# Performance work log

Hardware: AMD Instinct MI355X
Metric: run time of the kernel (lower is better)

The kernel has to match this reference:

```python
import jax, jax.numpy as jnp
import numpy as np

DIM, HEADS, MLP_RATIO = 384, 6, 4.0
HEAD_DIM = DIM // HEADS
HID = int(DIM * MLP_RATIO)
EPS = 1e-5


def _layer_norm(x, g, b):
    m = jnp.mean(x, axis=-1, keepdims=True)
    v = jnp.mean(jnp.square(x - m), axis=-1, keepdims=True)
    return (x - m) * jax.lax.rsqrt(v + EPS) * g + b


def setup_inputs() -> dict:
    key = jax.random.key(0)
    ks = jax.random.split(key, 16)
    B, N, C = 4, 2048, DIM
    s = 0.02
    return {
        "x": jax.random.normal(ks[0], (B, N, C), dtype=jnp.float32),
        "ln1_g": jnp.ones((C,), jnp.float32),
        "ln1_b": jnp.zeros((C,), jnp.float32),
        "qkv_w": jax.random.normal(ks[1], (C, 3 * C), jnp.float32) * s,  # [in, out]
        "qkv_b": jnp.zeros((3 * C,), jnp.float32),
        "proj_w": jax.random.normal(ks[2], (C, C), jnp.float32) * s,
        "proj_b": jnp.zeros((C,), jnp.float32),
        "ln2_g": jnp.ones((C,), jnp.float32),
        "ln2_b": jnp.zeros((C,), jnp.float32),
        "fc1_w": jax.random.normal(ks[3], (C, HID), jnp.float32) * s,
        "fc1_b": jnp.zeros((HID,), jnp.float32),
        "fc2_w": jax.random.normal(ks[4], (HID, C), jnp.float32) * s,
        "fc2_b": jnp.zeros((C,), jnp.float32),
    }


def reference(x, ln1_g, ln1_b, qkv_w, qkv_b, proj_w, proj_b,
              ln2_g, ln2_b, fc1_w, fc1_b, fc2_w, fc2_b):
    B, N, C = x.shape
    scale = HEAD_DIM ** (-0.5)

    # --- attention branch (pre-norm) ---
    h = _layer_norm(x, ln1_g, ln1_b)
    qkv = (h @ qkv_w + qkv_b).reshape(B, N, 3, HEADS, HEAD_DIM)
    qkv = jnp.transpose(qkv, (2, 0, 3, 1, 4))  # [3, B, H, N, D]
    q, k, v = qkv[0], qkv[1], qkv[2]
    attn = jnp.einsum("bhnd,bhmd->bhnm", q, k) * scale
    attn = jax.nn.softmax(attn, axis=-1)
    out = jnp.einsum("bhnm,bhmd->bhnd", attn, v)
    out = jnp.transpose(out, (0, 2, 1, 3)).reshape(B, N, C)
    x = x + (out @ proj_w + proj_b)

    # --- MLP branch (pre-norm) ---
    h = _layer_norm(x, ln2_g, ln2_b)
    h = jax.nn.gelu(h @ fc1_w + fc1_b, approximate=False)
    x = x + (h @ fc2_w + fc2_b)
    return x
```

## Files before the change

### kernel.cpp

```cpp
#include <hip/hip_runtime.h>

typedef unsigned short u16;
typedef unsigned int u32;
typedef __bf16 bf16x8_t __attribute__((ext_vector_type(8)));
typedef float f32x4 __attribute__((ext_vector_type(4)));
typedef float f32x16 __attribute__((ext_vector_type(16)));

__device__ __forceinline__ u16 f2b(float f) {
  union { float f; u32 u; } v; v.f = f;
  u32 r = v.u + 0x7fffu + ((v.u >> 16) & 1u);
  return (u16)(r >> 16);
}

__device__ __forceinline__ u32 pkbf(float a, float b) {
  union { __bf16 h[2]; u32 u; } v;
  v.h[0] = (__bf16)a; v.h[1] = (__bf16)b;
  return v.u;
}

__device__ __forceinline__ size_t fmoff(int r, int c, int Kd) {
  return ((size_t)(r >> 4) * (Kd >> 3) + (c >> 3)) * 128 + (r & 15) * 8 + (c & 7);
}

__device__ __forceinline__ f32x4 mfma16(uint4 a, uint4 b, f32x4 c) {
  return __builtin_amdgcn_mfma_f32_16x16x32_bf16(
      __builtin_bit_cast(bf16x8_t, a), __builtin_bit_cast(bf16x8_t, b), c, 0, 0, 0);
}

__device__ __forceinline__ f32x16 mfma32(uint4 a, uint4 b, f32x16 c) {
  return __builtin_amdgcn_mfma_f32_32x32x16_bf16(
      __builtin_bit_cast(bf16x8_t, a), __builtin_bit_cast(bf16x8_t, b), c, 0, 0, 0);
}

__device__ __forceinline__ void plswap(u32& a, u32& b) {
  asm("v_permlane32_swap_b32 %0, %1" : "+v"(a), "+v"(b));
}

__device__ __forceinline__ void load_lds16(const void* g, void* l) {
  __builtin_amdgcn_global_load_lds(
      (const __attribute__((address_space(1))) unsigned int*)g,
      (__attribute__((address_space(3))) unsigned int*)l, 16, 0, 0);
}

template <int N>
__device__ __forceinline__ void waitvm() {
  if constexpr (N == 0) asm volatile("s_waitcnt vmcnt(0)" ::: "memory");
  else if constexpr (N == 4) asm volatile("s_waitcnt vmcnt(4)" ::: "memory");
  else if constexpr (N == 6) asm volatile("s_waitcnt vmcnt(6)" ::: "memory");
  else if constexpr (N == 8) asm volatile("s_waitcnt vmcnt(8)" ::: "memory");
  else asm volatile("s_waitcnt vmcnt(10)" ::: "memory");
}

__device__ __forceinline__ void ln_body(const float* __restrict__ x,
                                        const float* __restrict__ g,
                                        const float* __restrict__ bta,
                                        u16* __restrict__ out, int row,
                                        int lane) {
  const float* xr = x + (size_t)row * 384;
  float v[6];
  float s = 0.f;
#pragma unroll
  for (int i = 0; i < 6; i++) { v[i] = xr[i * 64 + lane]; s += v[i]; }
#pragma unroll
  for (int off = 32; off >= 1; off >>= 1) s += __shfl_xor(s, off);
  float mean = s * (1.0f / 384.0f);
  float vs = 0.f;
#pragma unroll
  for (int i = 0; i < 6; i++) { float d = v[i] - mean; vs += d * d; }
#pragma unroll
  for (int off = 32; off >= 1; off >>= 1) vs += __shfl_xor(vs, off);
  float rstd = rsqrtf(vs * (1.0f / 384.0f) + 1e-5f);
#pragma unroll
  for (int i = 0; i < 6; i++) {
    int c = i * 64 + lane;
    out[fmoff(row, c, 384)] = f2b((v[i] - mean) * rstd * g[c] + bta[c]);
  }
}

__global__ __launch_bounds__(256) void ln_k(const float* __restrict__ x,
                                            const float* __restrict__ g,
                                            const float* __restrict__ bta,
                                            u16* __restrict__ out) {
  ln_body(x, g, bta, out, blockIdx.x * 4 + (threadIdx.x >> 6),
          threadIdx.x & 63);
}

__global__ __launch_bounds__(256) void prep_k(
    const float* __restrict__ w0, u16* __restrict__ t0_,
    const float* __restrict__ w1, u16* __restrict__ t1_,
    const float* __restrict__ w2, u16* __restrict__ t2_,
    const float* __restrict__ w3, u16* __restrict__ t3_,
    const float* __restrict__ x, const float* __restrict__ g,
    const float* __restrict__ bta, u16* __restrict__ lnout) {
  __shared__ u16 L[64][68];
  int tile = blockIdx.x, tid = threadIdx.x;
  if (tile >= 432) {
    ln_body(x, g, bta, lnout, (tile - 432) * 4 + (tid >> 6), tid & 63);
    return;
  }
  const float* w; u16* wt; int K, N, rel; bool fm;
  if (tile < 108)      { w = w0; wt = t0_; K = 384;  N = 1152; rel = tile;       fm = false; }
  else if (tile < 144) { w = w1; wt = t1_; K = 384;  N = 384;  rel = tile - 108; fm = true; }
  else if (tile < 288) { w = w2; wt = t2_; K = 384;  N = 1536; rel = tile - 144; fm = false; }
  else                 { w = w3; wt = t3_; K = 1536; N = 384;  rel = tile - 288; fm = true; }
  int ntx = N >> 6;
  int tk = (rel / ntx) << 6, tn = (rel - (rel / ntx) * ntx) << 6;

  int r = tid >> 2, c0 = (tid & 3) << 4;
  const float* src = w + (size_t)(tk + r) * N + tn + c0;
#pragma unroll
  for (int j = 0; j < 16; j += 4) {
    float4 a = *(const float4*)(src + j);
    L[r][c0 + j + 0] = f2b(a.x);
    L[r][c0 + j + 1] = f2b(a.y);
    L[r][c0 + j + 2] = f2b(a.z);
    L[r][c0 + j + 3] = f2b(a.w);
  }
  __syncthreads();
  int n = tid >> 2, k0 = (tid & 3) << 4;
  u16 tmp[16];
#pragma unroll
  for (int j = 0; j < 16; j++) tmp[j] = L[k0 + j][n];
  if (fm) {
    u16* dst = wt + fmoff(tn + n, tk + k0, K);
    *(uint4*)dst = *(const uint4*)(tmp);
    *(uint4*)(dst + 128) = *(const uint4*)(tmp + 8);
  } else {
    u16* dst = wt + (size_t)(tn + n) * K + tk + k0;
    *(uint4*)dst = *(const uint4*)(tmp);
    *(uint4*)(dst + 8) = *(const uint4*)(tmp + 8);
  }
}

template <int EPI, int MR, int KD, int NX, int MINW>
__global__ __launch_bounds__(256, MINW) void gemm_k(
    const u16* __restrict__ A, const u16* __restrict__ Bt,
    const float* __restrict__ bias, const float* __restrict__ res,
    void* __restrict__ outp, int Nn,
    u16* __restrict__ qp, u16* __restrict__ kp, u16* __restrict__ vtp) {
  constexpr int NS = KD / 64;
  constexpr int KD8 = KD / 8;
  __shared__ __align__(16) u16 Bs[3][64 * 64];
  int tid = threadIdx.x;
  int lane = tid & 63, wid = tid >> 6;
  int li = lane & 15, lg = lane >> 4;
  int wr = wid >> 1, wc = wid & 1;

  int p = blockIdx.x;
  int idx = p >> 3;
  int cx = idx % NX;
  int row0 = ((p & 7) + ((idx / NX) << 3)) * (MR * 32);
  int col0 = cx * 64;

  int lr = lane >> 3;
  int sc8 = ((lane & 7) ^ lr) * 8;

  const u16* Ab = A + ((size_t)(row0 / 16 + wr * MR) * KD8 + lg) * 128 + li * 8;

  f32x4 z = {0.f, 0.f, 0.f, 0.f};
  f32x4 acc[MR][2];
#pragma unroll
  for (int m = 0; m < MR; m++)
#pragma unroll
    for (int n = 0; n < 2; n++) acc[m][n] = z;

  uint4 af0[MR][2], af1[MR][2];

  auto stageB = [&](int buf, int k0) {
#pragma unroll
    for (int j = 0; j < 2; j++) {
      int ib = wid * 2 + j;
      load_lds16(Bt + (size_t)(col0 + ib * 8 + lr) * KD + k0 + sc8,
                 (char*)Bs[buf] + ib * 1024);
    }
  };
  auto loadA = [&](uint4 (*dst)[2], int t) {
#pragma unroll
    for (int m = 0; m < MR; m++)
#pragma unroll
      for (int kk = 0; kk < 2; kk++)
        dst[m][kk] =
            *(const uint4*)(Ab + ((size_t)m * KD8 + t * 8 + kk * 4) * 128);
  };

  stageB(0, 0);
  stageB(1, 64);
  loadA(af0, 0);
  if (NS > 1) loadA(af1, 1);
  waitvm<2 * MR>();
  __builtin_amdgcn_s_barrier();
  asm volatile("" ::: "memory");

#pragma unroll
  for (int t = 0; t < NS; t++) {
    if (t + 2 < NS) stageB((t + 2) % 3, (t + 2) * 64);
    const char* Bsb = (const char*)Bs[t % 3];
#pragma unroll
    for (int kk = 0; kk < 2; kk++) {
      uint4 bf[2];
#pragma unroll
      for (int n = 0; n < 2; n++) {
        int c = wc * 32 + n * 16 + li;
        bf[n] = *(const uint4*)(Bsb + c * 128 +
                                ((kk * 64 + lg * 16) ^ ((c & 7) << 4)));
      }
#pragma unroll
      for (int m = 0; m < MR; m++)
#pragma unroll
        for (int n = 0; n < 2; n++)
          acc[m][n] = mfma16((t & 1) ? af1[m][kk] : af0[m][kk], bf[n],
                             acc[m][n]);
    }
    if (t + 2 < NS) {
      if (t & 1) loadA(af1, t + 2);
      else       loadA(af0, t + 2);
      waitvm<2 + 2 * MR>();
      __builtin_amdgcn_s_barrier();
      asm volatile("" ::: "memory");
    } else if (t + 1 < NS) {
      waitvm<0>();
      __builtin_amdgcn_s_barrier();
      asm volatile("" ::: "memory");
    }
  }

#pragma unroll
  for (int m = 0; m < MR; m++) {
#pragma unroll
    for (int n = 0; n < 2; n++) {
#pragma unroll
      for (int j = 0; j < 4; j++) {
        int r = row0 + wr * (MR * 16) + m * 16 + lg * 4 + j;
        int c = col0 + wc * 32 + n * 16 + li;
        float v = acc[m][n][j] + bias[c];
        if (EPI == 1) {
          float e = __expf(-1.5957691f * v * (1.f + 0.044715f * v * v));
          ((u16*)outp)[fmoff(r, c, Nn)] = f2b(v / (1.f + e));
        } else {
          int tt = c / 384;
          int c2 = c - tt * 384;
          int hh = c2 >> 6, d = c2 & 63;
          int bb = r >> 11, nn = r & 2047;
          size_t bh = (size_t)bb * 6 + hh;
          int tile = nn >> 5;
          if (tt == 2) {
            int kvl = nn & 31;
            int kvHalf = (kvl >> 4) & 1, h2 = (kvl >> 3) & 1, jj = kvl & 7;
            int dTile = d >> 5, l31 = d & 31;
            vtp[(((bh * 64 + tile) * 2 + dTile) * 2 + kvHalf) * 512 +
                (l31 + h2 * 32) * 8 + jj] = f2b(v);
          } else {
            int chunk = d >> 4, h2 = (d >> 3) & 1, e = d & 7;
            int l31 = nn & 31;
            size_t off = ((bh * 64 + tile) * 4 + chunk) * 512 +
                         (l31 + h2 * 32) * 8 + e;
            if (tt == 0) qp[off] = f2b(v * 0.18033688f);
            else         kp[off] = f2b(v);
          }
        }
      }
    }
  }
}

template <int KD, int NX, int MINW>
__global__ __launch_bounds__(256, MINW) void gemm_thin_k(
    const u16* __restrict__ A, const u16* __restrict__ Bt,
    const float* __restrict__ bias, const float* __restrict__ res,
    float* __restrict__ outp, int Nn) {
  constexpr int NS = KD / 64;
  constexpr int KD8 = KD / 8;
  int tid = threadIdx.x;
  int lane = tid & 63, wid = tid >> 6;
  int li = lane & 15, lg = lane >> 4;
  int wr = wid >> 1, wc = wid & 1;

  int p = blockIdx.x;
  int idx = p >> 3;
  int cx = idx % NX;
  int row0 = ((p & 7) + ((idx / NX) << 3)) * 64;
  int col0 = cx * 64;

  const u16* Ab = A + ((size_t)(row0 / 16 + wr * 2) * KD8 + lg) * 128 + li * 8;
  const u16* Bb = Bt + ((size_t)(col0 / 16 + wc * 2) * KD8 + lg) * 128 + li * 8;

  f32x4 z = {0.f, 0.f, 0.f, 0.f};
  f32x4 acc[2][2];
#pragma unroll
  for (int m = 0; m < 2; m++)
#pragma unroll
    for (int n = 0; n < 2; n++) acc[m][n] = z;

  uint4 af0[2][2], af1[2][2], bf0[2][2], bf1[2][2];

  auto loadA = [&](uint4 (*dst)[2], int t) {
#pragma unroll
    for (int m = 0; m < 2; m++)
#pragma unroll
      for (int kk = 0; kk < 2; kk++)
        dst[m][kk] =
            *(const uint4*)(Ab + ((size_t)m * KD8 + t * 8 + kk * 4) * 128);
  };
  auto loadB = [&](uint4 (*dst)[2], int t) {
#pragma unroll
    for (int n = 0; n < 2; n++)
#pragma unroll
      for (int kk = 0; kk < 2; kk++)
        dst[n][kk] =
            *(const uint4*)(Bb + ((size_t)n * KD8 + t * 8 + kk * 4) * 128);
  };

  loadA(af0, 0);
  loadB(bf0, 0);

#pragma unroll
  for (int t = 0; t < NS; t++) {
    if (t + 1 < NS) {
      if (t & 1) { loadA(af0, t + 1); loadB(bf0, t + 1); }
      else       { loadA(af1, t + 1); loadB(bf1, t + 1); }
    }
#pragma unroll
    for (int kk = 0; kk < 2; kk++)
#pragma unroll
      for (int m = 0; m < 2; m++)
#pragma unroll
        for (int n = 0; n < 2; n++)
          acc[m][n] = mfma16((t & 1) ? af1[m][kk] : af0[m][kk],
                             (t & 1) ? bf1[n][kk] : bf0[n][kk], acc[m][n]);
  }

#pragma unroll
  for (int m = 0; m < 2; m++)
#pragma unroll
    for (int n = 0; n < 2; n++)
#pragma unroll
      for (int j = 0; j < 4; j++) {
        int r = row0 + wr * 32 + m * 16 + lg * 4 + j;
        int c = col0 + wc * 32 + n * 16 + li;
        float v = acc[m][n][j] + bias[c];
        outp[(size_t)r * Nn + c] = v + res[(size_t)r * Nn + c];
      }
}

__global__ __launch_bounds__(256, 2) void attn_k(const u16* __restrict__ q,
                                                 const u16* __restrict__ k,
                                                 const u16* __restrict__ vt,
                                                 u16* __restrict__ out) {
  __shared__ __align__(16) float Ol[3][2][16][64];
  __shared__ float Ls[3][64];

  int tid = threadIdx.x;
  int lane = tid & 63, wid = tid >> 6;
  int l31 = lane & 31, hi = lane >> 5;
  int bid = blockIdx.x;
  int nid = (bid & 7) * 96 + (bid >> 3);
  int bh = nid >> 5, qT = nid & 31;
  int b = bh / 6, hh = bh - b * 6;
  int qb = qT * 64;

  const u16* qp_ = q + ((size_t)bh * 64 + qT * 2) * 2048 + lane * 8;
  const u16* kp_ = k + ((size_t)bh * 64 + wid * 16) * 2048 + lane * 8;
  const u16* vp_ = vt + ((size_t)bh * 64 + wid * 16) * 2048 + lane * 8;

  uint4 qf0[4], qf1[4], kf[4];
#pragma unroll
  for (int c = 0; c < 4; c++) qf0[c] = *(const uint4*)(qp_ + c * 512);
#pragma unroll
  for (int c = 0; c < 4; c++) qf1[c] = *(const uint4*)(qp_ + 2048 + c * 512);
#pragma unroll
  for (int c = 0; c < 4; c++) kf[c] = *(const uint4*)(kp_ + c * 512);
  kp_ += 2048;

  f32x16 o00, o01, o10, o11;
#pragma unroll
  for (int r = 0; r < 16; r++) {
    o00[r] = 0.f; o01[r] = 0.f; o10[r] = 0.f; o11[r] = 0.f;
  }
  float ls0 = 0.f, ls1 = 0.f;

#pragma unroll
  for (int t = 0; t < 16; t++) {
    uint4 vf0 = *(const uint4*)(vp_);
    uint4 vf1 = *(const uint4*)(vp_ + 512);
    uint4 vf2 = *(const uint4*)(vp_ + 1024);
    uint4 vf3 = *(const uint4*)(vp_ + 1536);
    uint4 kn[4];
    if (t < 15) {
#pragma unroll
      for (int c = 0; c < 4; c++) kn[c] = *(const uint4*)(kp_ + c * 512);
    }

    {
      f32x16 s;
#pragma unroll
      for (int r = 0; r < 16; r++) s[r] = 0.f;
#pragma unroll
      for (int c = 0; c < 4; c++) s = mfma32(kf[c], qf0[c], s);
      float p[16];
#pragma unroll
      for (int r = 0; r < 16; r++) p[r] = __builtin_amdgcn_exp2f(s[r]);
      ls0 += ((p[0] + p[1]) + (p[2] + p[3])) + ((p[4] + p[5]) + (p[6] + p[7])) +
             ((p[8] + p[9]) + (p[10] + p[11])) +
             ((p[12] + p[13]) + (p[14] + p[15]));
      u32 u[8];
#pragma unroll
      for (int i = 0; i < 8; i++) u[i] = pkbf(p[2 * i], p[2 * i + 1]);
      plswap(u[0], u[2]); plswap(u[1], u[3]);
      plswap(u[4], u[6]); plswap(u[5], u[7]);
      uint4 pa0 = {u[0], u[1], u[2], u[3]};
      uint4 pa1 = {u[4], u[5], u[6], u[7]};
      o00 = mfma32(pa0, vf0, o00);
      o00 = mfma32(pa1, vf1, o00);
      o01 = mfma32(pa0, vf2, o01);
      o01 = mfma32(pa1, vf3, o01);
    }
    {
      f32x16 s;
#pragma unroll
      for (int r = 0; r < 16; r++) s[r] = 0.f;
#pragma unroll
      for (int c = 0; c < 4; c++) s = mfma32(kf[c], qf1[c], s);
      float p[16];
#pragma unroll
      for (int r = 0; r < 16; r++) p[r] = __builtin_amdgcn_exp2f(s[r]);
      ls1 += ((p[0] + p[1]) + (p[2] + p[3])) + ((p[4] + p[5]) + (p[6] + p[7])) +
             ((p[8] + p[9]) + (p[10] + p[11])) +
             ((p[12] + p[13]) + (p[14] + p[15]));
      u32 u[8];
#pragma unroll
      for (int i = 0; i < 8; i++) u[i] = pkbf(p[2 * i], p[2 * i + 1]);
      plswap(u[0], u[2]); plswap(u[1], u[3]);
      plswap(u[4], u[6]); plswap(u[5], u[7]);
      uint4 pa0 = {u[0], u[1], u[2], u[3]};
      uint4 pa1 = {u[4], u[5], u[6], u[7]};
      o10 = mfma32(pa0, vf0, o10);
      o10 = mfma32(pa1, vf1, o10);
      o11 = mfma32(pa0, vf2, o11);
      o11 = mfma32(pa1, vf3, o11);
    }

    if (t < 15) {
#pragma unroll
      for (int c = 0; c < 4; c++) kf[c] = kn[c];
    }
    kp_ += 2048;
    vp_ += 2048;
  }

  ls0 += __shfl_xor(ls0, 32);
  ls1 += __shfl_xor(ls1, 32);

  if (wid) {
#pragma unroll
    for (int r = 0; r < 16; r++) {
      Ol[wid - 1][0][r][lane] = o00[r];
      Ol[wid - 1][1][r][lane] = o01[r];
    }
    Ls[wid - 1][lane] = ls0;
  }
  __syncthreads();
  if (wid == 0) {
#pragma unroll
    for (int w = 0; w < 3; w++) ls0 += Ls[w][lane];
#pragma unroll
    for (int r = 0; r < 16; r++)
#pragma unroll
      for (int w = 0; w < 3; w++) {
        o00[r] += Ol[w][0][r][lane];
        o01[r] += Ol[w][1][r][lane];
      }
    float rl = 1.0f / ls0;
#pragma unroll
    for (int r = 0; r < 16; r++) {
      int qo = (r & 3) + 8 * (r >> 2) + hi * 4;
      float rlq = __shfl(rl, qo, 64);
      int row = b * 2048 + qb + qo;
      out[fmoff(row, hh * 64 + l31, 384)] = f2b(o00[r] * rlq);
      out[fmoff(row, hh * 64 + 32 + l31, 384)] = f2b(o01[r] * rlq);
    }
  }
  __syncthreads();
  if (wid) {
#pragma unroll
    for (int r = 0; r < 16; r++) {
      Ol[wid - 1][0][r][lane] = o10[r];
      Ol[wid - 1][1][r][lane] = o11[r];
    }
    Ls[wid - 1][lane] = ls1;
  }
  __syncthreads();
  if (wid == 0) {
#pragma unroll
    for (int w = 0; w < 3; w++) ls1 += Ls[w][lane];
#pragma unroll
    for (int r = 0; r < 16; r++)
#pragma unroll
      for (int w = 0; w < 3; w++) {
        o10[r] += Ol[w][0][r][lane];
        o11[r] += Ol[w][1][r][lane];
      }
    float rl = 1.0f / ls1;
#pragma unroll
    for (int r = 0; r < 16; r++) {
      int qo = (r & 3) + 8 * (r >> 2) + hi * 4;
      float rlq = __shfl(rl, qo, 64);
      int row = b * 2048 + qb + 32 + qo;
      out[fmoff(row, hh * 64 + l31, 384)] = f2b(o10[r] * rlq);
      out[fmoff(row, hh * 64 + 32 + l31, 384)] = f2b(o11[r] * rlq);
    }
  }
}

extern "C" void kernel_launch(void* const* d_in, const int* in_sizes, int n_in,
                              void* d_out, int out_size, void* d_ws,
                              size_t ws_size, hipStream_t stream) {
  const float* x      = (const float*)d_in[0];
  const float* ln1_g  = (const float*)d_in[1];
  const float* ln1_b  = (const float*)d_in[2];
  const float* qkv_w  = (const float*)d_in[3];
  const float* qkv_b  = (const float*)d_in[4];
  const float* proj_w = (const float*)d_in[5];
  const float* proj_b = (const float*)d_in[6];
  const float* ln2_g  = (const float*)d_in[7];
  const float* ln2_b  = (const float*)d_in[8];
  const float* fc1_w  = (const float*)d_in[9];
  const float* fc1_b  = (const float*)d_in[10];
  const float* fc2_w  = (const float*)d_in[11];
  const float* fc2_b  = (const float*)d_in[12];
  float* out = (float*)d_out;

  char* p = (char*)d_ws;
  u16* qkvwt  = (u16*)p;  p += (size_t)1152 * 384 * 2;
  u16* projwt = (u16*)p;  p += (size_t)384 * 384 * 2;
  u16* fc1wt  = (u16*)p;  p += (size_t)1536 * 384 * 2;
  u16* fc2wt  = (u16*)p;  p += (size_t)384 * 1536 * 2;
  float* x1   = (float*)p; p += (size_t)8192 * 384 * 4;
  u16* reg1   = (u16*)p;  p += (size_t)8192 * 384 * 2;
  u16* reg2   = (u16*)p;  p += (size_t)8192 * 1536 * 2;
  u16* qd  = reg2;
  u16* kd  = reg2 + (size_t)24 * 2048 * 64;
  u16* vtd = kd + (size_t)24 * 2048 * 64;
  u16* h3  = reg2;

  prep_k<<<432 + 2048, 256, 0, stream>>>(qkv_w, qkvwt, proj_w, projwt,
                                         fc1_w, fc1wt, fc2_w, fc2wt,
                                         x, ln1_g, ln1_b, reg1);
  gemm_k<2, 4, 384, 18, 2><<<dim3(1152), 256, 0, stream>>>(
      reg1, qkvwt, qkv_b, nullptr, nullptr, 1152, qd, kd, vtd);
  attn_k<<<dim3(768), 256, 0, stream>>>(qd, kd, vtd, reg1);
  gemm_thin_k<384, 6, 4><<<dim3(768), 256, 0, stream>>>(
      reg1, projwt, proj_b, x, x1, 384);
  ln_k<<<2048, 256, 0, stream>>>(x1, ln2_g, ln2_b, reg1);
  gemm_k<1, 4, 384, 24, 2><<<dim3(1536), 256, 0, stream>>>(
      reg1, fc1wt, fc1_b, nullptr, h3, 1536, nullptr, nullptr, nullptr);
  gemm_thin_k<1536, 6, 4><<<dim3(768), 256, 0, stream>>>(
      h3, fc2wt, fc2_b, x1, out, 384);
}
```

Measured before the change: 124.6 us.

## Fuse projection GEMM, residual and LayerNorm2; route fc2 through generic gemm kernel

Replaces the thin projection GEMM and the separate LN2 kernel with one projln_k kernel. Each block computes 16 full 384-wide rows, adds bias and residual, writes x1, and computes the LayerNorm statistics through shuffles and shared memory before emitting the bf16 LN output. This removes one launch and the re-read of x1 from global memory. The fc2 GEMM now uses the general gemm_k template with a new fp32 residual epilogue, and the fc2 weight prep layout flag changes to match. The single-pass E[x^2]-mean^2 variance is less numerically robust, and the narrower row tiles cut weight reuse per block.

Measured after the change: 121.4 us. -2.6%, faster.

```diff
diff --git a/kernel.cpp b/kernel.cpp
--- a/kernel.cpp
+++ b/kernel.cpp
@@ -75,14 +75,6 @@
     int c = i * 64 + lane;
     out[fmoff(row, c, 384)] = f2b((v[i] - mean) * rstd * g[c] + bta[c]);
   }
-}
-
-__global__ __launch_bounds__(256) void ln_k(const float* __restrict__ x,
-                                            const float* __restrict__ g,
-                                            const float* __restrict__ bta,
-                                            u16* __restrict__ out) {
-  ln_body(x, g, bta, out, blockIdx.x * 4 + (threadIdx.x >> 6),
-          threadIdx.x & 63);
 }
 
 __global__ __launch_bounds__(256) void prep_k(
@@ -102,7 +94,7 @@
   if (tile < 108)      { w = w0; wt = t0_; K = 384;  N = 1152; rel = tile;       fm = false; }
   else if (tile < 144) { w = w1; wt = t1_; K = 384;  N = 384;  rel = tile - 108; fm = true; }
   else if (tile < 288) { w = w2; wt = t2_; K = 384;  N = 1536; rel = tile - 144; fm = false; }
-  else                 { w = w3; wt = t3_; K = 1536; N = 384;  rel = tile - 288; fm = true; }
+  else                 { w = w3; wt = t3_; K = 1536; N = 384;  rel = tile - 288; fm = false; }
   int ntx = N >> 6;
   int tk = (rel / ntx) << 6, tn = (rel - (rel / ntx) * ntx) << 6;
 
@@ -233,7 +225,9 @@
         int r = row0 + wr * (MR * 16) + m * 16 + lg * 4 + j;
         int c = col0 + wc * 32 + n * 16 + li;
         float v = acc[m][n][j] + bias[c];
-        if (EPI == 1) {
+        if (EPI == 0) {
+          ((float*)outp)[(size_t)r * Nn + c] = v + res[(size_t)r * Nn + c];
+        } else if (EPI == 1) {
           float e = __expf(-1.5957691f * v * (1.f + 0.044715f * v * v));
           ((u16*)outp)[fmoff(r, c, Nn)] = f2b(v / (1.f + e));
         } else {
@@ -263,83 +257,107 @@
   }
 }
 
-template <int KD, int NX, int MINW>
-__global__ __launch_bounds__(256, MINW) void gemm_thin_k(
+__global__ __launch_bounds__(256, 2) void projln_k(
     const u16* __restrict__ A, const u16* __restrict__ Bt,
-    const float* __restrict__ bias, const float* __restrict__ res,
-    float* __restrict__ outp, int Nn) {
-  constexpr int NS = KD / 64;
-  constexpr int KD8 = KD / 8;
+    const float* __restrict__ bias, const float* __restrict__ x,
+    const float* __restrict__ g2, const float* __restrict__ b2,
+    float* __restrict__ x1, u16* __restrict__ h2) {
+  __shared__ float Sm[4][16], Sv[4][16];
   int tid = threadIdx.x;
   int lane = tid & 63, wid = tid >> 6;
   int li = lane & 15, lg = lane >> 4;
-  int wr = wid >> 1, wc = wid & 1;
-
-  int p = blockIdx.x;
-  int idx = p >> 3;
-  int cx = idx % NX;
-  int row0 = ((p & 7) + ((idx / NX) << 3)) * 64;
-  int col0 = cx * 64;
-
-  const u16* Ab = A + ((size_t)(row0 / 16 + wr * 2) * KD8 + lg) * 128 + li * 8;
-  const u16* Bb = Bt + ((size_t)(col0 / 16 + wc * 2) * KD8 + lg) * 128 + li * 8;
+  int r0 = blockIdx.x * 16;
+
+  const u16* Ab = A + ((size_t)(r0 >> 4) * 48 + lg) * 128 + li * 8;
+  const u16* Bb = Bt + ((size_t)(wid * 6) * 48 + lg) * 128 + li * 8;
 
   f32x4 z = {0.f, 0.f, 0.f, 0.f};
-  f32x4 acc[2][2];
-#pragma unroll
-  for (int m = 0; m < 2; m++)
-#pragma unroll
-    for (int n = 0; n < 2; n++) acc[m][n] = z;
-
-  uint4 af0[2][2], af1[2][2], bf0[2][2], bf1[2][2];
-
-  auto loadA = [&](uint4 (*dst)[2], int t) {
-#pragma unroll
-    for (int m = 0; m < 2; m++)
-#pragma unroll
-      for (int kk = 0; kk < 2; kk++)
-        dst[m][kk] =
-            *(const uint4*)(Ab + ((size_t)m * KD8 + t * 8 + kk * 4) * 128);
+  f32x4 acc[6];
+#pragma unroll
+  for (int n = 0; n < 6; n++) acc[n] = z;
+
+  uint4 af0[2], af1[2], bf0[6][2], bf1[6][2];
+  auto loadA = [&](uint4* dst, int t) {
+#pragma unroll
+    for (int kk = 0; kk < 2; kk++)
+      dst[kk] = *(const uint4*)(Ab + ((size_t)t * 8 + kk * 4) * 128);
   };
   auto loadB = [&](uint4 (*dst)[2], int t) {
 #pragma unroll
-    for (int n = 0; n < 2; n++)
+    for (int n = 0; n < 6; n++)
 #pragma unroll
       for (int kk = 0; kk < 2; kk++)
         dst[n][kk] =
-            *(const uint4*)(Bb + ((size_t)n * KD8 + t * 8 + kk * 4) * 128);
+            *(const uint4*)(Bb + ((size_t)n * 48 + t * 8 + kk * 4) * 128);
   };
 
   loadA(af0, 0);
   loadB(bf0, 0);
-
-#pragma unroll
-  for (int t = 0; t < NS; t++) {
-    if (t + 1 < NS) {
+#pragma unroll
+  for (int t = 0; t < 6; t++) {
+    if (t + 1 < 6) {
       if (t & 1) { loadA(af0, t + 1); loadB(bf0, t + 1); }
       else       { loadA(af1, t + 1); loadB(bf1, t + 1); }
     }
 #pragma unroll
     for (int kk = 0; kk < 2; kk++)
 #pragma unroll
-      for (int m = 0; m < 2; m++)
-#pragma unroll
-        for (int n = 0; n < 2; n++)
-          acc[m][n] = mfma16((t & 1) ? af1[m][kk] : af0[m][kk],
-                             (t & 1) ? bf1[n][kk] : bf0[n][kk], acc[m][n]);
-  }
-
-#pragma unroll
-  for (int m = 0; m < 2; m++)
-#pragma unroll
-    for (int n = 0; n < 2; n++)
-#pragma unroll
-      for (int j = 0; j < 4; j++) {
-        int r = row0 + wr * 32 + m * 16 + lg * 4 + j;
-        int c = col0 + wc * 32 + n * 16 + li;
-        float v = acc[m][n][j] + bias[c];
-        outp[(size_t)r * Nn + c] = v + res[(size_t)r * Nn + c];
-      }
+      for (int n = 0; n < 6; n++)
+        acc[n] = mfma16((t & 1) ? af1[kk] : af0[kk],
+                        (t & 1) ? bf1[n][kk] : bf0[n][kk], acc[n]);
+  }
+
+  float vv[6][4];
+  float s1[4] = {0.f, 0.f, 0.f, 0.f}, s2[4] = {0.f, 0.f, 0.f, 0.f};
+#pragma unroll
+  for (int n = 0; n < 6; n++) {
+    int c = wid * 96 + n * 16 + li;
+    float bc = bias[c];
+#pragma unroll
+    for (int j = 0; j < 4; j++) {
+      int r = r0 + lg * 4 + j;
+      float v = acc[n][j] + bc + x[(size_t)r * 384 + c];
+      vv[n][j] = v;
+      x1[(size_t)r * 384 + c] = v;
+      s1[j] += v;
+      s2[j] += v * v;
+    }
+  }
+#pragma unroll
+  for (int off = 8; off >= 1; off >>= 1)
+#pragma unroll
+    for (int j = 0; j < 4; j++) {
+      s1[j] += __shfl_xor(s1[j], off);
+      s2[j] += __shfl_xor(s2[j], off);
+    }
+  if (li == 0) {
+#pragma unroll
+    for (int j = 0; j < 4; j++) {
+      Sm[wid][lg * 4 + j] = s1[j];
+      Sv[wid][lg * 4 + j] = s2[j];
+    }
+  }
+  __syncthreads();
+  float mean[4], rstd[4];
+#pragma unroll
+  for (int j = 0; j < 4; j++) {
+    int rr = lg * 4 + j;
+    float t1 = (Sm[0][rr] + Sm[1][rr]) + (Sm[2][rr] + Sm[3][rr]);
+    float t2 = (Sv[0][rr] + Sv[1][rr]) + (Sv[2][rr] + Sv[3][rr]);
+    float m = t1 * (1.0f / 384.0f);
+    mean[j] = m;
+    rstd[j] = rsqrtf(t2 * (1.0f / 384.0f) - m * m + 1e-5f);
+  }
+#pragma unroll
+  for (int n = 0; n < 6; n++) {
+    int c = wid * 96 + n * 16 + li;
+    float gc = g2[c], bc = b2[c];
+#pragma unroll
+    for (int j = 0; j < 4; j++) {
+      int r = r0 + lg * 4 + j;
+      h2[fmoff(r, c, 384)] = f2b((vv[n][j] - mean[j]) * rstd[j] * gc + bc);
+    }
+  }
 }
 
 __global__ __launch_bounds__(256, 2) void attn_k(const u16* __restrict__ q,
@@ -548,11 +566,10 @@
   gemm_k<2, 4, 384, 18, 2><<<dim3(1152), 256, 0, stream>>>(
       reg1, qkvwt, qkv_b, nullptr, nullptr, 1152, qd, kd, vtd);
   attn_k<<<dim3(768), 256, 0, stream>>>(qd, kd, vtd, reg1);
-  gemm_thin_k<384, 6, 4><<<dim3(768), 256, 0, stream>>>(
-      reg1, projwt, proj_b, x, x1, 384);
-  ln_k<<<2048, 256, 0, stream>>>(x1, ln2_g, ln2_b, reg1);
+  projln_k<<<dim3(512), 256, 0, stream>>>(reg1, projwt, proj_b, x,
+                                          ln2_g, ln2_b, x1, reg1);
   gemm_k<1, 4, 384, 24, 2><<<dim3(1536), 256, 0, stream>>>(
       reg1, fc1wt, fc1_b, nullptr, h3, 1536, nullptr, nullptr, nullptr);
-  gemm_thin_k<1536, 6, 4><<<dim3(768), 256, 0, stream>>>(
-      h3, fc2wt, fc2_b, x1, out, 384);
-}
+  gemm_k<0, 2, 1536, 6, 4><<<dim3(768), 256, 0, stream>>>(
+      h3, fc2wt, fc2_b, x1, out, 384, nullptr, nullptr, nullptr);
+}
```
